# Optimization experiments

Hardware: AMD Instinct MI355X
Metric: run time of the kernel (lower is better)

Reference implementation:

```python
import jax, jax.numpy as jnp
import numpy as np

LN_EPS = 1e-5

def _layernorm(x, g, b):
    mu = jnp.mean(x, axis=-1, keepdims=True)
    var = jnp.mean(jnp.square(x - mu), axis=-1, keepdims=True)
    return (x - mu) * jax.lax.rsqrt(var + LN_EPS) * g + b

def setup_inputs() -> dict:
    key = jax.random.key(0)
    B, T, C = 8, 2048, 1024
    ks = jax.random.split(key, 16)
    s = 1.0 / np.sqrt(C)
    inp = {
        'x':   jax.random.normal(ks[0], (B, T, C), dtype=jnp.float32),
        'Wq':  jax.random.uniform(ks[1], (C, C), jnp.float32, -s, s),
        'bq':  jax.random.uniform(ks[2], (C,), jnp.float32, -s, s),
        'Wk':  jax.random.uniform(ks[3], (C, C), jnp.float32, -s, s),
        'bk':  jax.random.uniform(ks[4], (C,), jnp.float32, -s, s),
        'Wv':  jax.random.uniform(ks[5], (C, C), jnp.float32, -s, s),
        'bv':  jax.random.uniform(ks[6], (C,), jnp.float32, -s, s),
        'g1':  jnp.ones((C,), jnp.float32),
        'be1': jnp.zeros((C,), jnp.float32),
        'W1':  jax.random.uniform(ks[7], (C, C), jnp.float32, -s, s),
        'bf1': jax.random.uniform(ks[8], (C,), jnp.float32, -s, s),
        'W2':  jax.random.uniform(ks[9], (C, C), jnp.float32, -s, s),
        'bf2': jax.random.uniform(ks[10], (C,), jnp.float32, -s, s),
        'g2':  jnp.ones((C,), jnp.float32),
        'be2': jnp.zeros((C,), jnp.float32),
    }
    return inp

def reference(x, Wq, bq, Wk, bk, Wv, bv, g1, be1, W1, bf1, W2, bf2, g2, be2):
    B, T, C = x.shape
    q = x @ Wq + bq
    k = x @ Wk + bk
    v = x @ Wv + bv
    # FFT cross-correlation along time axis
    fq = jnp.fft.rfft(q, axis=1)
    fk = jnp.fft.rfft(k, axis=1)
    corr = jnp.fft.irfft(fq * jnp.conj(fk), n=T, axis=1)  # [B,T,C]
    weights = jax.nn.softmax(corr, axis=1)
    # einsum 'btd,btv->btd': weights * sum over v's channel dim
    attn = weights * jnp.sum(v, axis=-1, keepdims=True)
    x = _layernorm(x + attn, g1, be1)
    h = jax.nn.relu(x @ W1 + bf1) @ W2 + bf2
    x = _layernorm(x + h, g2, be2)
    return x
```

## Files before the change

### kernel.cpp

```cpp
#include <hip/hip_runtime.h>
#include <math.h>

#define B_DIM 8
#define T_DIM 2048
#define C_DIM 1024
#define BT_DIM (B_DIM * T_DIM)
#define FSZ ((size_t)BT_DIM * C_DIM)
#define LN_EPS 1e-5f

typedef __bf16 bf16x8 __attribute__((ext_vector_type(8)));
typedef _Float16 f16x8 __attribute__((ext_vector_type(8)));
typedef float f32x4 __attribute__((ext_vector_type(4)));

__device__ __forceinline__ unsigned short f2bf(float f) {
  __bf16 h = (__bf16)f;
  return __builtin_bit_cast(unsigned short, h);
}
__device__ __forceinline__ unsigned short f2h(float f) {
  _Float16 h = (_Float16)f;
  return __builtin_bit_cast(unsigned short, h);
}

__device__ __forceinline__ void gld16(const void* g, void* l) {
  __builtin_amdgcn_global_load_lds(
      (const __attribute__((address_space(1))) unsigned int*)g,
      (__attribute__((address_space(3))) unsigned int*)l, 16, 0, 0);
}

__device__ __forceinline__ int swz(int a) {
  return a ^ (((a >> 4) ^ (a >> 8)) & 15);
}

__device__ __forceinline__ int enc11(int f) {
  return ((f & 3) << 9) | (((f >> 2) & 3) << 7) | (((f >> 4) & 3) << 5) |
         (((f >> 6) & 3) << 3) | (((f >> 8) & 3) << 1) | ((f >> 10) & 1);
}

__global__ __launch_bounds__(256)
void cvt_split_f16_kernel(const float* __restrict__ x, unsigned short* __restrict__ hi,
                          unsigned short* __restrict__ lo) {
  size_t idx = ((size_t)blockIdx.x * 256 + threadIdx.x) * 4;
  float4 v = *(const float4*)(x + idx);
  float f[4] = {v.x, v.y, v.z, v.w};
  unsigned short hv[4], lv[4];
#pragma unroll
  for (int i = 0; i < 4; i++) {
    _Float16 hb = (_Float16)f[i];
    hv[i] = __builtin_bit_cast(unsigned short, hb);
    lv[i] = f2h(f[i] - (float)hb);
  }
  *(ushort4*)(hi + idx) = make_ushort4(hv[0], hv[1], hv[2], hv[3]);
  *(ushort4*)(lo + idx) = make_ushort4(lv[0], lv[1], lv[2], lv[3]);
}

__global__ __launch_bounds__(256)
void wtrans_f16_kernel(const float* __restrict__ W, unsigned short* __restrict__ Wt,
                       int K, int N) {
  __shared__ float tile[32][33];
  const int tid = threadIdx.x;
  const int tx = tid & 31, ty = tid >> 5;
  const int n0 = blockIdx.x * 32, k0 = blockIdx.y * 32;
#pragma unroll
  for (int i = 0; i < 4; i++) {
    int row = ty + i * 8;
    tile[row][tx] = W[(size_t)(k0 + row) * N + n0 + tx];
  }
  __syncthreads();
#pragma unroll
  for (int i = 0; i < 4; i++) {
    int row = ty + i * 8;
    Wt[(size_t)(n0 + row) * K + k0 + tx] = f2h(tile[tx][row]);
  }
}

__global__ __launch_bounds__(256)
void wtrans_kernel(const float* __restrict__ W, unsigned short* __restrict__ Wt,
                   int K, int N) {
  __shared__ float tile[32][33];
  const int tid = threadIdx.x;
  const int tx = tid & 31, ty = tid >> 5;
  const int n0 = blockIdx.x * 32, k0 = blockIdx.y * 32;
#pragma unroll
  for (int i = 0; i < 4; i++) {
    int row = ty + i * 8;
    tile[row][tx] = W[(size_t)(k0 + row) * N + n0 + tx];
  }
  __syncthreads();
#pragma unroll
  for (int i = 0; i < 4; i++) {
    int row = ty + i * 8;
    Wt[(size_t)(n0 + row) * K + k0 + tx] = f2bf(tile[tx][row]);
  }
}

__global__ __launch_bounds__(256)
void wv_rowsum_kernel(const float* __restrict__ Wv, const float* __restrict__ bv,
                      float* __restrict__ wvsum, float* __restrict__ bvsum) {
  const int r = blockIdx.x;
  const int tid = threadIdx.x;
  const float* src = (r < C_DIM) ? (Wv + (size_t)r * C_DIM) : bv;
  float4 t4 = *(const float4*)(src + (tid << 2));
  float s = t4.x + t4.y + t4.z + t4.w;
#pragma unroll
  for (int off = 32; off > 0; off >>= 1) s += __shfl_down(s, off);
  __shared__ float ps[4];
  if ((tid & 63) == 0) ps[tid >> 6] = s;
  __syncthreads();
  if (tid == 0) {
    float v = ps[0] + ps[1] + ps[2] + ps[3];
    if (r < C_DIM) wvsum[r] = v; else bvsum[0] = v;
  }
}

__global__ __launch_bounds__(256)
void sv_dot_kernel(const float* __restrict__ x, const float* __restrict__ wvsum,
                   const float* __restrict__ bvsum, float* __restrict__ sv) {
  const int r = blockIdx.x;
  const int tid = threadIdx.x;
  float4 a = *(const float4*)(x + (size_t)r * C_DIM + (tid << 2));
  float4 w = *(const float4*)(wvsum + (tid << 2));
  float s = a.x * w.x + a.y * w.y + a.z * w.z + a.w * w.w;
#pragma unroll
  for (int off = 32; off > 0; off >>= 1) s += __shfl_down(s, off);
  __shared__ float ps[4];
  if ((tid & 63) == 0) ps[tid >> 6] = s;
  __syncthreads();
  if (tid == 0) sv[r] = ps[0] + ps[1] + ps[2] + ps[3] + bvsum[0];
}

__global__ __launch_bounds__(256, 2)
void gemm_bf16_kernel(const __bf16* __restrict__ A, const __bf16* __restrict__ Bt,
                      const float* __restrict__ bias, float* Yf, unsigned short* Yb,
                      int K, int N, int do_relu) {
  __shared__ __align__(16) __bf16 As[128 * 32];
  __shared__ __align__(16) __bf16 Bs[128 * 32];
  const int tid = threadIdx.x;
  const int wave = tid >> 6, lane = tid & 63;
  const int wr = wave >> 1, wc = wave & 1;
  const int r15 = lane & 15, kq = lane >> 4;
  const int m0 = blockIdx.y * 128, n0 = blockIdx.x * 128;

  f32x4 acc[4][4] = {};

  for (int k0 = 0; k0 < K; k0 += 32) {
#pragma unroll
    for (int r = 0; r < 2; ++r) {
      int idx = r * 256 + tid;
      int row = idx >> 2;
      int ko = (idx & 3) ^ ((row >> 1) & 3);
      gld16(A + (size_t)(m0 + row) * K + k0 + ko * 8, &As[idx * 8]);
      gld16(Bt + (size_t)(n0 + row) * K + k0 + ko * 8, &Bs[idx * 8]);
    }
    __syncthreads();
    bf16x8 afr[4], bfr[4];
#pragma unroll
    for (int i = 0; i < 4; i++) {
      int ar = wr * 64 + i * 16 + r15;
      afr[i] = *(const bf16x8*)&As[(ar * 4 + (kq ^ ((ar >> 1) & 3))) * 8];
      int br = wc * 64 + i * 16 + r15;
      bfr[i] = *(const bf16x8*)&Bs[(br * 4 + (kq ^ ((br >> 1) & 3))) * 8];
    }
#pragma unroll
    for (int mi = 0; mi < 4; mi++)
#pragma unroll
      for (int ni = 0; ni < 4; ni++)
        acc[mi][ni] = __builtin_amdgcn_mfma_f32_16x16x32_bf16(afr[mi], bfr[ni], acc[mi][ni], 0, 0, 0);
    __syncthreads();
  }

  float bv[4];
#pragma unroll
  for (int ni = 0; ni < 4; ni++) bv[ni] = bias[n0 + wc * 64 + ni * 16 + r15];

#pragma unroll
  for (int mi = 0; mi < 4; mi++)
#pragma unroll
    for (int ni = 0; ni < 4; ni++) {
      const int n = n0 + wc * 64 + ni * 16 + r15;
#pragma unroll
      for (int r = 0; r < 4; r++) {
        const int m = m0 + wr * 64 + mi * 16 + kq * 4 + r;
        float v = acc[mi][ni][r] + bv[ni];
        if (do_relu) v = fmaxf(v, 0.f);
        if (Yf) Yf[(size_t)m * N + n] = v;
        if (Yb) Yb[(size_t)m * N + n] = f2bf(v);
      }
    }
}

__global__ __launch_bounds__(512, 2)
void gemm_qkT_f16_8ph_kernel(const _Float16* __restrict__ Ahi, const _Float16* __restrict__ Alo,
                             const _Float16* __restrict__ Bq, const _Float16* __restrict__ Bk,
                             const float* __restrict__ biasq, const float* __restrict__ biask,
                             float* __restrict__ Yq, float* __restrict__ Yk, int K, int N) {
  __shared__ __align__(16) _Float16 AhL[3][256 * 32];
  __shared__ __align__(16) _Float16 AlL[3][256 * 32];
  __shared__ __align__(16) _Float16 BqL[3][128 * 32];
  __shared__ __align__(16) _Float16 BkL[3][128 * 32];

  const int tid = threadIdx.x;
  const int wave = tid >> 6, lane = tid & 63;
  const int wr = wave >> 2, wc = wave & 3;
  const int r15 = lane & 15, kq = lane >> 4;
  const int m0 = blockIdx.y * 256, n0 = blockIdx.x * 128;
  const int NT = K >> 5;

  const int row_a0 = tid >> 2;
  const int row_a1 = row_a0 + 128;
  const int ch = tid & 3;
  const int ko0 = ch ^ ((row_a0 >> 1) & 3);
  const int ko1 = ch ^ ((row_a1 >> 1) & 3);
  const _Float16* agh0 = Ahi + (size_t)(m0 + row_a0) * K + ko0 * 8;
  const _Float16* agl0 = Alo + (size_t)(m0 + row_a0) * K + ko0 * 8;
  const _Float16* agh1 = Ahi + (size_t)(m0 + row_a1) * K + ko1 * 8;
  const _Float16* agl1 = Alo + (size_t)(m0 + row_a1) * K + ko1 * 8;
  const _Float16* bgq  = Bq  + (size_t)(n0 + row_a0) * K + ko0 * 8;
  const _Float16* bgk  = Bk  + (size_t)(n0 + row_a0) * K + ko0 * 8;

  const int ksel = kq ^ ((r15 >> 1) & 3);
  const int aoff = (wr * 128 + r15) * 32 + ksel * 8;
  const int boff = (wc * 32 + r15) * 32 + ksel * 8;

  f32x4 accq[8][2] = {};
  f32x4 acck[8][2] = {};

  gld16(agh0 + 0, &AhL[0][(size_t)tid * 8]);
  gld16(agl0 + 0, &AlL[0][(size_t)tid * 8]);
  gld16(agh1 + 0, &AhL[0][(size_t)(tid + 512) * 8]);
  gld16(agl1 + 0, &AlL[0][(size_t)(tid + 512) * 8]);
  gld16(bgq + 0, &BqL[0][(size_t)tid * 8]);
  gld16(bgk + 0, &BkL[0][(size_t)tid * 8]);
  gld16(agh0 + 32, &AhL[1][(size_t)tid * 8]);
  gld16(agl0 + 32, &AlL[1][(size_t)tid * 8]);
  gld16(agh1 + 32, &AhL[1][(size_t)(tid + 512) * 8]);
  gld16(agl1 + 32, &AlL[1][(size_t)(tid + 512) * 8]);
  gld16(bgq + 32, &BqL[1][(size_t)tid * 8]);
  gld16(bgk + 32, &BkL[1][(size_t)tid * 8]);

  int bR = 0;
  int bS = 2;

  for (int j = 0; j < NT; ++j) {
    if (j < NT - 1) {
      asm volatile("s_waitcnt vmcnt(6)" ::: "memory");
    } else {
      asm volatile("s_waitcnt vmcnt(0)" ::: "memory");
    }
    __builtin_amdgcn_s_barrier();
    __builtin_amdgcn_sched_barrier(0);

    const int kk = (j + 2) * 32;
    const bool doStage = (j + 2 < NT);

    f16x8 bqf[2], bkf[2];
#pragma unroll
    for (int ni = 0; ni < 2; ++ni) {
      bqf[ni] = *(const f16x8*)&BqL[bR][boff + ni * 512];
      bkf[ni] = *(const f16x8*)&BkL[bR][boff + ni * 512];
    }

#pragma unroll
    for (int p = 0; p < 4; ++p) {
      f16x8 ah0 = *(const f16x8*)&AhL[bR][aoff + (2 * p + 0) * 512];
      f16x8 al0 = *(const f16x8*)&AlL[bR][aoff + (2 * p + 0) * 512];
      f16x8 ah1 = *(const f16x8*)&AhL[bR][aoff + (2 * p + 1) * 512];
      f16x8 al1 = *(const f16x8*)&AlL[bR][aoff + (2 * p + 1) * 512];
      if (doStage) {
        if (p == 0) {
          gld16(agh0 + kk, &AhL[bS][(size_t)tid * 8]);
          gld16(agl0 + kk, &AlL[bS][(size_t)tid * 8]);
        }
        if (p == 1) {
          gld16(agh1 + kk, &AhL[bS][(size_t)(tid + 512) * 8]);
          gld16(agl1 + kk, &AlL[bS][(size_t)(tid + 512) * 8]);
        }
        if (p == 2) gld16(bgq + kk, &BqL[bS][(size_t)tid * 8]);
        if (p == 3) gld16(bgk + kk, &BkL[bS][(size_t)tid * 8]);
      }
      __builtin_amdgcn_s_barrier();
      asm volatile("s_waitcnt lgkmcnt(0)" ::: "memory");
      __builtin_amdgcn_sched_barrier(0);
      __builtin_amdgcn_s_setprio(1);
#pragma unroll
      for (int m2 = 0; m2 < 2; ++m2) {
        const int mi = 2 * p + m2;
        const f16x8 ahv = m2 ? ah1 : ah0;
        const f16x8 alv = m2 ? al1 : al0;
#pragma unroll
        for (int ni = 0; ni < 2; ++ni) {
          accq[mi][ni] = __builtin_amdgcn_mfma_f32_16x16x32_f16(ahv, bqf[ni], accq[mi][ni], 0, 0, 0);
          accq[mi][ni] = __builtin_amdgcn_mfma_f32_16x16x32_f16(alv, bqf[ni], accq[mi][ni], 0, 0, 0);
          acck[mi][ni] = __builtin_amdgcn_mfma_f32_16x16x32_f16(ahv, bkf[ni], acck[mi][ni], 0, 0, 0);
          acck[mi][ni] = __builtin_amdgcn_mfma_f32_16x16x32_f16(alv, bkf[ni], acck[mi][ni], 0, 0, 0);
        }
      }
      __builtin_amdgcn_s_setprio(0);
      __builtin_amdgcn_sched_barrier(0);
    }

    bR = (bR + 1 == 3) ? 0 : bR + 1;
    bS = (bS + 1 == 3) ? 0 : bS + 1;
  }

  float bvq[2], bvk[2];
#pragma unroll
  for (int ni = 0; ni < 2; ++ni) {
    bvq[ni] = biasq[n0 + wc * 32 + ni * 16 + r15];
    bvk[ni] = biask[n0 + wc * 32 + ni * 16 + r15];
  }

#pragma unroll
  for (int mi = 0; mi < 8; ++mi) {
    const int mbase = m0 + wr * 128 + mi * 16 + kq * 4;
    const int bb = mbase >> 11;
    const int t = mbase & (T_DIM - 1);
#pragma unroll
    for (int ni = 0; ni < 2; ++ni) {
      const int n = n0 + wc * 32 + ni * 16 + r15;
      const size_t o = ((size_t)bb * C_DIM + n) * T_DIM + t;
      *(float4*)(Yq + o) = make_float4(accq[mi][ni][0] + bvq[ni], accq[mi][ni][1] + bvq[ni],
                                       accq[mi][ni][2] + bvq[ni], accq[mi][ni][3] + bvq[ni]);
      *(float4*)(Yk + o) = make_float4(acck[mi][ni][0] + bvk[ni], acck[mi][ni][1] + bvk[ni],
                                       acck[mi][ni][2] + bvk[ni], acck[mi][ni][3] + bvk[ni]);
    }
  }
}

__device__ void fft_dif(float2* X, const float2* tw, int tid, float sgn) {
#pragma unroll
  for (int s = 0; s < 5; s++) {
    const int m = 512 >> (2 * s);
    const int jstep = 512 / m;
#pragma unroll
    for (int ii = 0; ii < 2; ii++) {
      const int i = tid + ii * 256;
      const int q = i & (m - 1);
      const int a0 = ((i - q) << 2) + q;
      float2 x0 = X[swz(a0)];
      float2 x1 = X[swz(a0 + m)];
      float2 x2 = X[swz(a0 + 2 * m)];
      float2 x3 = X[swz(a0 + 3 * m)];
      float2 t0 = make_float2(x0.x + x2.x, x0.y + x2.y);
      float2 t2 = make_float2(x0.x - x2.x, x0.y - x2.y);
      float2 t1 = make_float2(x1.x + x3.x, x1.y + x3.y);
      float2 t3 = make_float2(x1.x - x3.x, x1.y - x3.y);
      const float jx = -sgn * t3.y, jy = sgn * t3.x;
      float2 y0 = make_float2(t0.x + t1.x, t0.y + t1.y);
      float2 y1 = make_float2(t2.x + jx, t2.y + jy);
      float2 y2 = make_float2(t0.x - t1.x, t0.y - t1.y);
      float2 y3 = make_float2(t2.x - jx, t2.y - jy);
      const int j1 = q * jstep;
      float2 tv = tw[swz(j1)];
      const float c1 = tv.x, s1 = tv.y * sgn;
      const float c2 = c1 * c1 - s1 * s1, s2 = 2.f * c1 * s1;
      const float c3 = c2 * c1 - s2 * s1, s3 = c2 * s1 + s2 * c1;
      X[swz(a0)] = y0;
      X[swz(a0 + m)] = make_float2(c1 * y1.x - s1 * y1.y, c1 * y1.y + s1 * y1.x);
      X[swz(a0 + 2 * m)] = make_float2(c2 * y2.x - s2 * y2.y, c2 * y2.y + s2 * y2.x);
      X[swz(a0 + 3 * m)] = make_float2(c3 * y3.x - s3 * y3.y, c3 * y3.y + s3 * y3.x);
    }
    __syncthreads();
  }
#pragma unroll
  for (int ii = 0; ii < 4; ii++) {
    const int a = (tid + ii * 256) << 1;
    float2 u = X[swz(a)], v = X[swz(a + 1)];
    X[swz(a)] = make_float2(u.x + v.x, u.y + v.y);
    X[swz(a + 1)] = make_float2(u.x - v.x, u.y - v.y);
  }
  __syncthreads();
}

__device__ void fft_dit_inv(float2* X, const float2* tw, int tid) {
#pragma unroll
  for (int ii = 0; ii < 4; ii++) {
    const int a = (tid + ii * 256) << 1;
    float2 u = X[swz(a)], v = X[swz(a + 1)];
    X[swz(a)] = make_float2(u.x + v.x, u.y + v.y);
    X[swz(a + 1)] = make_float2(u.x - v.x, u.y - v.y);
  }
  __syncthreads();
#pragma unroll
  for (int s = 4; s >= 0; s--) {
    const int m = 512 >> (2 * s);
    const int jstep = 512 / m;
#pragma unroll
    for (int ii = 0; ii < 2; ii++) {
      const int i = tid + ii * 256;
      const int q = i & (m - 1);
      const int a0 = ((i - q) << 2) + q;
      float2 v0 = X[swz(a0)];
      float2 v1 = X[swz(a0 + m)];
      float2 v2 = X[swz(a0 + 2 * m)];
      float2 v3 = X[swz(a0 + 3 * m)];
      const int j1 = q * jstep;
      float2 tv = tw[swz(j1)];
      const float c1 = tv.x, s1 = tv.y;
      const float c2 = c1 * c1 - s1 * s1, s2 = 2.f * c1 * s1;
      const float c3 = c2 * c1 - s2 * s1, s3 = c2 * s1 + s2 * c1;
      float2 w1 = make_float2(c1 * v1.x - s1 * v1.y, c1 * v1.y + s1 * v1.x);
      float2 w2 = make_float2(c2 * v2.x - s2 * v2.y, c2 * v2.y + s2 * v2.x);
      float2 w3 = make_float2(c3 * v3.x - s3 * v3.y, c3 * v3.y + s3 * v3.x);
      float2 t0 = make_float2(v0.x + w2.x, v0.y + w2.y);
      float2 t2 = make_float2(v0.x - w2.x, v0.y - w2.y);
      float2 t1 = make_float2(w1.x + w3.x, w1.y + w3.y);
      float2 t3 = make_float2(w1.x - w3.x, w1.y - w3.y);
      const float jx = -t3.y, jy = t3.x;
      X[swz(a0)] = make_float2(t0.x + t1.x, t0.y + t1.y);
      X[swz(a0 + m)] = make_float2(t2.x + jx, t2.y + jy);
      X[swz(a0 + 2 * m)] = make_float2(t0.x - t1.x, t0.y - t1.y);
      X[swz(a0 + 3 * m)] = make_float2(t2.x - jx, t2.y - jy);
    }
    __syncthreads();
  }
}

__global__ __launch_bounds__(256)
void corr_fft_kernel(const float* qT, const float* kT, float* corrT,
                     float* __restrict__ Mv, float* __restrict__ Iv) {
  __shared__ float2 bA[2048];
  __shared__ float2 bB[2048];
  __shared__ float2 tw[512];
  __shared__ float2 red[4];
  const int tid = threadIdx.x;
  const int wave = tid >> 6, lane = tid & 63;
  const int b = blockIdx.y;
  const int c0 = blockIdx.x * 2;
  const float* q0 = qT + ((size_t)b * C_DIM + c0) * T_DIM;
  const float* k0p = kT + ((size_t)b * C_DIM + c0) * T_DIM;

#pragma unroll
  for (int jj = 0; jj < 2; jj++) {
    int j = tid + jj * 256;
    float sA, cA;
    __sincosf((float)j * (6.283185307179586f / 2048.0f), &sA, &cA);
    tw[swz(j)] = make_float2(cA, sA);
  }

#pragma unroll
  for (int jj = 0; jj < 8; jj++) {
    int t = tid + jj * 256;
    bA[swz(t)] = make_float2(q0[t], q0[t + T_DIM]);
    bB[swz(t)] = make_float2(k0p[t], k0p[t + T_DIM]);
  }
  __syncthreads();

  fft_dif(bA, tw, tid, -1.0f);
  fft_dif(bB, tw, tid, -1.0f);

#pragma unroll 1
  for (int f = tid; f <= 1024; f += 256) {
    const int g = (2048 - f) & 2047;
    const int p = swz(enc11(f));
    const int p2 = swz(enc11(g));
    float2 Zq = bA[p], Zq2 = bA[p2];
    float2 Zk = bB[p], Zk2 = bB[p2];
    float2 Aq = make_float2(0.5f * (Zq.x + Zq2.x), 0.5f * (Zq.y - Zq2.y));
    float2 Dq = make_float2(Zq.x - Zq2.x, Zq.y + Zq2.y);
    float2 Bq = make_float2(0.5f * Dq.y, -0.5f * Dq.x);
    float2 Ak = make_float2(0.5f * (Zk.x + Zk2.x), 0.5f * (Zk.y - Zk2.y));
    float2 Dk = make_float2(Zk.x - Zk2.x, Zk.y + Zk2.y);
    float2 Bk = make_float2(0.5f * Dk.y, -0.5f * Dk.x);
    float2 G = make_float2(Aq.x * Ak.x + Aq.y * Ak.y, Aq.y * Ak.x - Aq.x * Ak.y);
    float2 H = make_float2(Bq.x * Bk.x + Bq.y * Bk.y, Bq.y * Bk.x - Bq.x * Bk.y);
    bA[p] = make_float2(G.x - H.y, G.y + H.x);
    if (p2 != p) bA[p2] = make_float2(G.x + H.y, -G.y + H.x);
  }
  __syncthreads();

  fft_dit_inv(bA, tw, tid);

  float* o0 = corrT + ((size_t)b * C_DIM + c0) * T_DIM;
  const float sc = 1.0f / 2048.0f;
  float mx0 = -INFINITY, mx1 = -INFINITY;
#pragma unroll
  for (int jj = 0; jj < 8; jj++) {
    int t = tid + jj * 256;
    float2 o = bA[swz(t)];
    float v0 = o.x * sc, v1 = o.y * sc;
    o0[t] = v0;
    o0[t + T_DIM] = v1;
    mx0 = fmaxf(mx0, v0);
    mx1 = fmaxf(mx1, v1);
  }
#pragma unroll
  for (int off = 32; off > 0; off >>= 1) {
    mx0 = fmaxf(mx0, __shfl_down(mx0, off));
    mx1 = fmaxf(mx1, __shfl_down(mx1, off));
  }
  if (lane == 0) red[wave] = make_float2(mx0, mx1);
  __syncthreads();
  const float M0 = fmaxf(fmaxf(red[0].x, red[1].x), fmaxf(red[2].x, red[3].x));
  const float M1 = fmaxf(fmaxf(red[0].y, red[1].y), fmaxf(red[2].y, red[3].y));
  __syncthreads();
  float s0 = 0.f, s1 = 0.f;
#pragma unroll
  for (int jj = 0; jj < 8; jj++) {
    int t = tid + jj * 256;
    float2 o = bA[swz(t)];
    s0 += __expf(o.x * sc - M0);
    s1 += __expf(o.y * sc - M1);
  }
#pragma unroll
  for (int off = 32; off > 0; off >>= 1) {
    s0 += __shfl_down(s0, off);
    s1 += __shfl_down(s1, off);
  }
  if (lane == 0) red[wave] = make_float2(s0, s1);
  __syncthreads();
  if (tid == 0) {
    float S0 = red[0].x + red[1].x + red[2].x + red[3].x;
    float S1 = red[0].y + red[1].y + red[2].y + red[3].y;
    Mv[(size_t)b * C_DIM + c0] = M0;
    Mv[(size_t)b * C_DIM + c0 + 1] = M1;
    Iv[(size_t)b * C_DIM + c0] = 1.0f / S0;
    Iv[(size_t)b * C_DIM + c0 + 1] = 1.0f / S1;
  }
}

__global__ __launch_bounds__(256)
void attn_transpose_kernel(const float* __restrict__ corrT, const float* __restrict__ Mv,
                           const float* __restrict__ Iv, const float* __restrict__ sv,
                           float* __restrict__ attn) {
  __shared__ float tile[32][33];
  const int tid = threadIdx.x;
  const int tx = tid & 31, ty = tid >> 5;
  const int t0 = blockIdx.x * 32, c0 = blockIdx.y * 32, b = blockIdx.z;
  const float svv = sv[(size_t)b * T_DIM + t0 + tx];
#pragma unroll
  for (int i = 0; i < 4; i++) {
    const int c = c0 + ty + i * 8;
    const float M = Mv[(size_t)b * C_DIM + c];
    const float I = Iv[(size_t)b * C_DIM + c];
    float v = corrT[((size_t)b * C_DIM + c) * T_DIM + t0 + tx];
    tile[ty + i * 8][tx] = __expf(v - M) * I * svv;
  }
  __syncthreads();
#pragma unroll
  for (int i = 0; i < 4; i++) {
    const int t = t0 + ty + i * 8;
    attn[((size_t)b * T_DIM + t) * C_DIM + c0 + tx] = tile[tx][ty + i * 8];
  }
}

__global__ __launch_bounds__(256)
void add_ln_kernel(const float* __restrict__ A, const float* __restrict__ Bv,
                   const float* __restrict__ g, const float* __restrict__ be,
                   float* __restrict__ outf, unsigned short* outb) {
  const int r = blockIdx.x;
  const int tid = threadIdx.x;
  const size_t base = (size_t)r * C_DIM + (tid << 2);
  float4 a = *(const float4*)(A + base);
  float4 b = *(const float4*)(Bv + base);
  float x0 = a.x + b.x, x1 = a.y + b.y, x2 = a.z + b.z, x3 = a.w + b.w;
  float s = x0 + x1 + x2 + x3;
  float s2 = x0 * x0 + x1 * x1 + x2 * x2 + x3 * x3;
#pragma unroll
  for (int off = 32; off > 0; off >>= 1) {
    s += __shfl_down(s, off);
    s2 += __shfl_down(s2, off);
  }
  __shared__ float ps[4], ps2[4];
  if ((tid & 63) == 0) { ps[tid >> 6] = s; ps2[tid >> 6] = s2; }
  __syncthreads();
  float S = ps[0] + ps[1] + ps[2] + ps[3];
  float S2 = ps2[0] + ps2[1] + ps2[2] + ps2[3];
  const float mu = S * (1.0f / C_DIM);
  const float var = S2 * (1.0f / C_DIM) - mu * mu;
  const float rs = rsqrtf(var + LN_EPS);
  float4 gv = *(const float4*)(g + (tid << 2));
  float4 bev = *(const float4*)(be + (tid << 2));
  float o0 = (x0 - mu) * rs * gv.x + bev.x;
  float o1 = (x1 - mu) * rs * gv.y + bev.y;
  float o2 = (x2 - mu) * rs * gv.z + bev.z;
  float o3 = (x3 - mu) * rs * gv.w + bev.w;
  *(float4*)(outf + base) = make_float4(o0, o1, o2, o3);
  if (outb) *(ushort4*)(outb + base) = make_ushort4(f2bf(o0), f2bf(o1), f2bf(o2), f2bf(o3));
}

extern "C" void kernel_launch(void* const* d_in, const int* in_sizes, int n_in,
                              void* d_out, int out_size, void* d_ws, size_t ws_size,
                              hipStream_t stream) {
  const float* x   = (const float*)d_in[0];
  const float* Wq  = (const float*)d_in[1];
  const float* bq  = (const float*)d_in[2];
  const float* Wk  = (const float*)d_in[3];
  const float* bk  = (const float*)d_in[4];
  const float* Wv  = (const float*)d_in[5];
  const float* bv  = (const float*)d_in[6];
  const float* g1  = (const float*)d_in[7];
  const float* be1 = (const float*)d_in[8];
  const float* W1  = (const float*)d_in[9];
  const float* bf1 = (const float*)d_in[10];
  const float* W2  = (const float*)d_in[11];
  const float* bf2 = (const float*)d_in[12];
  const float* g2  = (const float*)d_in[13];
  const float* be2 = (const float*)d_in[14];
  float* out = (float*)d_out;

  float* ws = (float*)d_ws;
  float* qbuf = ws;
  float* kbuf = ws + FSZ;
  unsigned short* xhi = (unsigned short*)(ws + 2 * FSZ);
  unsigned short* xlo = xhi + FSZ;
  unsigned short* wA = xlo + FSZ;
  unsigned short* wB = wA + (size_t)C_DIM * C_DIM;
  float* sv = (float*)(wB + (size_t)C_DIM * C_DIM);
  float* wvsum = sv + BT_DIM;
  float* bvsum = wvsum + C_DIM;
  float* Mv = bvsum + 1;
  float* Iv = Mv + (size_t)B_DIM * C_DIM;

  const dim3 blk(256);
  const dim3 ggrid(C_DIM / 128, BT_DIM / 128);
  const dim3 qkgrid(C_DIM / 128, BT_DIM / 256);
  const dim3 tgrid(C_DIM / 32, C_DIM / 32);

  cvt_split_f16_kernel<<<dim3(FSZ / 1024), blk, 0, stream>>>(x, xhi, xlo);

  wv_rowsum_kernel<<<dim3(C_DIM + 1), blk, 0, stream>>>(Wv, bv, wvsum, bvsum);
  sv_dot_kernel<<<dim3(BT_DIM), blk, 0, stream>>>(x, wvsum, bvsum, sv);

  wtrans_f16_kernel<<<tgrid, blk, 0, stream>>>(Wq, wA, C_DIM, C_DIM);
  wtrans_f16_kernel<<<tgrid, blk, 0, stream>>>(Wk, wB, C_DIM, C_DIM);
  gemm_qkT_f16_8ph_kernel<<<qkgrid, dim3(512), 0, stream>>>(
      (const _Float16*)xhi, (const _Float16*)xlo,
      (const _Float16*)wA, (const _Float16*)wB,
      bq, bk, qbuf, kbuf, C_DIM, C_DIM);

  corr_fft_kernel<<<dim3(C_DIM / 2, B_DIM), blk, 0, stream>>>(qbuf, kbuf, qbuf, Mv, Iv);

  attn_transpose_kernel<<<dim3(T_DIM / 32, C_DIM / 32, B_DIM), blk, 0, stream>>>(
      qbuf, Mv, Iv, sv, kbuf);

  add_ln_kernel<<<dim3(BT_DIM), blk, 0, stream>>>(x, kbuf, g1, be1, qbuf, xhi);

  wtrans_kernel<<<tgrid, blk, 0, stream>>>(W1, wA, C_DIM, C_DIM);
  wtrans_kernel<<<tgrid, blk, 0, stream>>>(W2, wB, C_DIM, C_DIM);

  gemm_bf16_kernel<<<ggrid, blk, 0, stream>>>((const __bf16*)xhi, (const __bf16*)wA,
                                              bf1, nullptr, xlo, C_DIM, C_DIM, 1);
  gemm_bf16_kernel<<<ggrid, blk, 0, stream>>>((const __bf16*)xlo, (const __bf16*)wB,
                                              bf2, kbuf, nullptr, C_DIM, C_DIM, 0);

  add_ln_kernel<<<dim3(BT_DIM), blk, 0, stream>>>(qbuf, kbuf, g2, be2, out, nullptr);
}
```

Baseline: 581.7 us.

## Fuse sv dot into split conversion, attn into LN1, and remap GEMM tiles for XCD locality

The sv dot product now runs inside the fp16 hi/lo split kernel, so x is read once there instead of twice. The softmax-normalise/transpose pass is merged with the first residual add and LayerNorm, staging a 32x1024 tile in shared memory so the attn intermediate never goes to global memory. Both GEMM kernels remap block indices so each XCD works on a compact M/N region for better L2 reuse. The fused attn_ln kernel uses about 128KB of LDS per block, which limits occupancy, and its corrT reads are column-strided. Buffer roles for the second GEMM and the final LayerNorm are swapped to match.

```diff
diff --git a/kernel.cpp b/kernel.cpp
--- a/kernel.cpp
+++ b/kernel.cpp
@@ -37,10 +37,15 @@
 }
 
 __global__ __launch_bounds__(256)
-void cvt_split_f16_kernel(const float* __restrict__ x, unsigned short* __restrict__ hi,
-                          unsigned short* __restrict__ lo) {
-  size_t idx = ((size_t)blockIdx.x * 256 + threadIdx.x) * 4;
-  float4 v = *(const float4*)(x + idx);
+void cvt_split_sv_kernel(const float* __restrict__ x, const float* __restrict__ wvsum,
+                         const float* __restrict__ bvsum,
+                         unsigned short* __restrict__ hi, unsigned short* __restrict__ lo,
+                         float* __restrict__ sv) {
+  const int r = blockIdx.x;
+  const int tid = threadIdx.x;
+  const size_t base = (size_t)r * C_DIM + (tid << 2);
+  float4 v = *(const float4*)(x + base);
+  float4 w = *(const float4*)(wvsum + (tid << 2));
   float f[4] = {v.x, v.y, v.z, v.w};
   unsigned short hv[4], lv[4];
 #pragma unroll
@@ -49,8 +54,15 @@
     hv[i] = __builtin_bit_cast(unsigned short, hb);
     lv[i] = f2h(f[i] - (float)hb);
   }
-  *(ushort4*)(hi + idx) = make_ushort4(hv[0], hv[1], hv[2], hv[3]);
-  *(ushort4*)(lo + idx) = make_ushort4(lv[0], lv[1], lv[2], lv[3]);
+  *(ushort4*)(hi + base) = make_ushort4(hv[0], hv[1], hv[2], hv[3]);
+  *(ushort4*)(lo + base) = make_ushort4(lv[0], lv[1], lv[2], lv[3]);
+  float s = v.x * w.x + v.y * w.y + v.z * w.z + v.w * w.w;
+#pragma unroll
+  for (int off = 32; off > 0; off >>= 1) s += __shfl_down(s, off);
+  __shared__ float ps[4];
+  if ((tid & 63) == 0) ps[tid >> 6] = s;
+  __syncthreads();
+  if (tid == 0) sv[r] = ps[0] + ps[1] + ps[2] + ps[3] + bvsum[0];
 }
 
 __global__ __launch_bounds__(256)
@@ -110,22 +122,6 @@
     float v = ps[0] + ps[1] + ps[2] + ps[3];
     if (r < C_DIM) wvsum[r] = v; else bvsum[0] = v;
   }
-}
-
-__global__ __launch_bounds__(256)
-void sv_dot_kernel(const float* __restrict__ x, const float* __restrict__ wvsum,
-                   const float* __restrict__ bvsum, float* __restrict__ sv) {
-  const int r = blockIdx.x;
-  const int tid = threadIdx.x;
-  float4 a = *(const float4*)(x + (size_t)r * C_DIM + (tid << 2));
-  float4 w = *(const float4*)(wvsum + (tid << 2));
-  float s = a.x * w.x + a.y * w.y + a.z * w.z + a.w * w.w;
-#pragma unroll
-  for (int off = 32; off > 0; off >>= 1) s += __shfl_down(s, off);
-  __shared__ float ps[4];
-  if ((tid & 63) == 0) ps[tid >> 6] = s;
-  __syncthreads();
-  if (tid == 0) sv[r] = ps[0] + ps[1] + ps[2] + ps[3] + bvsum[0];
 }
 
 __global__ __launch_bounds__(256, 2)
@@ -138,7 +134,11 @@
   const int wave = tid >> 6, lane = tid & 63;
   const int wr = wave >> 1, wc = wave & 1;
   const int r15 = lane & 15, kq = lane >> 4;
-  const int m0 = blockIdx.y * 128, n0 = blockIdx.x * 128;
+  const int h = blockIdx.y * 8 + blockIdx.x;
+  const int xcd = h & 7, s = h >> 3;
+  const int mIdx = (xcd << 4) + (s & 7) + ((s >> 6) << 3);
+  const int nIdx = (s >> 3) & 7;
+  const int m0 = mIdx * 128, n0 = nIdx * 128;
 
   f32x4 acc[4][4] = {};
 
@@ -202,7 +202,11 @@
   const int wave = tid >> 6, lane = tid & 63;
   const int wr = wave >> 2, wc = wave & 3;
   const int r15 = lane & 15, kq = lane >> 4;
-  const int m0 = blockIdx.y * 256, n0 = blockIdx.x * 128;
+  const int h = blockIdx.y * 8 + blockIdx.x;
+  const int xcd = h & 7, s = h >> 3;
+  const int mIdx = (xcd << 3) + (s & 3) + ((s >> 5) << 2);
+  const int nIdx = (s >> 2) & 7;
+  const int m0 = mIdx * 256, n0 = nIdx * 128;
   const int NT = K >> 5;
 
   const int row_a0 = tid >> 2;
@@ -518,28 +522,70 @@
   }
 }
 
-__global__ __launch_bounds__(256)
-void attn_transpose_kernel(const float* __restrict__ corrT, const float* __restrict__ Mv,
-                           const float* __restrict__ Iv, const float* __restrict__ sv,
-                           float* __restrict__ attn) {
-  __shared__ float tile[32][33];
-  const int tid = threadIdx.x;
-  const int tx = tid & 31, ty = tid >> 5;
-  const int t0 = blockIdx.x * 32, c0 = blockIdx.y * 32, b = blockIdx.z;
-  const float svv = sv[(size_t)b * T_DIM + t0 + tx];
-#pragma unroll
-  for (int i = 0; i < 4; i++) {
-    const int c = c0 + ty + i * 8;
-    const float M = Mv[(size_t)b * C_DIM + c];
-    const float I = Iv[(size_t)b * C_DIM + c];
-    float v = corrT[((size_t)b * C_DIM + c) * T_DIM + t0 + tx];
-    tile[ty + i * 8][tx] = __expf(v - M) * I * svv;
-  }
-  __syncthreads();
-#pragma unroll
-  for (int i = 0; i < 4; i++) {
-    const int t = t0 + ty + i * 8;
-    attn[((size_t)b * T_DIM + t) * C_DIM + c0 + tx] = tile[tx][ty + i * 8];
+__global__ __launch_bounds__(512)
+void attn_ln_kernel(const float* __restrict__ corrT, const float* __restrict__ Mv,
+                    const float* __restrict__ Iv, const float* __restrict__ sv,
+                    const float* __restrict__ x, const float* __restrict__ g,
+                    const float* __restrict__ be, float* __restrict__ outf,
+                    unsigned short* __restrict__ outb) {
+  __shared__ float att[32][1028];
+  const int tid = threadIdx.x;
+  const int b = blockIdx.y;
+  const int t0 = blockIdx.x * 32;
+
+  const int tx = tid & 31;
+  const int cy = tid >> 5;
+  const float* cb = corrT + (size_t)b * C_DIM * T_DIM + t0 + tx;
+  const float* Mb = Mv + (size_t)b * C_DIM;
+  const float* Ib = Iv + (size_t)b * C_DIM;
+#pragma unroll 8
+  for (int it = 0; it < 64; ++it) {
+    const int c = cy + (it << 4);
+    float v = cb[(size_t)c * T_DIM];
+    att[tx][c] = __expf(v - Mb[c]) * Ib[c];
+  }
+  __syncthreads();
+
+  const int t = tid >> 4;
+  const int l16 = tid & 15;
+  const float svv = sv[(size_t)b * T_DIM + t0 + t];
+  const float* xr = x + ((size_t)b * T_DIM + t0 + t) * C_DIM;
+  float s = 0.f, s2 = 0.f;
+#pragma unroll
+  for (int j = 0; j < 16; ++j) {
+    const int c = (l16 + (j << 4)) << 2;
+    float4 xv = *(const float4*)(xr + c);
+    float4 av = *(const float4*)&att[t][c];
+    float v0 = xv.x + av.x * svv;
+    float v1 = xv.y + av.y * svv;
+    float v2 = xv.z + av.z * svv;
+    float v3 = xv.w + av.w * svv;
+    *(float4*)&att[t][c] = make_float4(v0, v1, v2, v3);
+    s += v0 + v1 + v2 + v3;
+    s2 += v0 * v0 + v1 * v1 + v2 * v2 + v3 * v3;
+  }
+#pragma unroll
+  for (int off = 8; off > 0; off >>= 1) {
+    s += __shfl_xor(s, off);
+    s2 += __shfl_xor(s2, off);
+  }
+  const float mu = s * (1.0f / C_DIM);
+  const float var = s2 * (1.0f / C_DIM) - mu * mu;
+  const float rs = rsqrtf(var + LN_EPS);
+  float* orow = outf + ((size_t)b * T_DIM + t0 + t) * C_DIM;
+  unsigned short* obrow = outb + ((size_t)b * T_DIM + t0 + t) * C_DIM;
+#pragma unroll
+  for (int j = 0; j < 16; ++j) {
+    const int c = (l16 + (j << 4)) << 2;
+    float4 val = *(const float4*)&att[t][c];
+    float4 gv = *(const float4*)(g + c);
+    float4 bev = *(const float4*)(be + c);
+    float o0 = (val.x - mu) * rs * gv.x + bev.x;
+    float o1 = (val.y - mu) * rs * gv.y + bev.y;
+    float o2 = (val.z - mu) * rs * gv.z + bev.z;
+    float o3 = (val.w - mu) * rs * gv.w + bev.w;
+    *(float4*)(orow + c) = make_float4(o0, o1, o2, o3);
+    *(ushort4*)(obrow + c) = make_ushort4(f2bf(o0), f2bf(o1), f2bf(o2), f2bf(o3));
   }
 }
 
@@ -616,10 +662,9 @@
   const dim3 qkgrid(C_DIM / 128, BT_DIM / 256);
   const dim3 tgrid(C_DIM / 32, C_DIM / 32);
 
-  cvt_split_f16_kernel<<<dim3(FSZ / 1024), blk, 0, stream>>>(x, xhi, xlo);
-
   wv_rowsum_kernel<<<dim3(C_DIM + 1), blk, 0, stream>>>(Wv, bv, wvsum, bvsum);
-  sv_dot_kernel<<<dim3(BT_DIM), blk, 0, stream>>>(x, wvsum, bvsum, sv);
+
+  cvt_split_sv_kernel<<<dim3(BT_DIM), blk, 0, stream>>>(x, wvsum, bvsum, xhi, xlo, sv);
 
   wtrans_f16_kernel<<<tgrid, blk, 0, stream>>>(Wq, wA, C_DIM, C_DIM);
   wtrans_f16_kernel<<<tgrid, blk, 0, stream>>>(Wk, wB, C_DIM, C_DIM);
@@ -630,10 +675,8 @@
 
   corr_fft_kernel<<<dim3(C_DIM / 2, B_DIM), blk, 0, stream>>>(qbuf, kbuf, qbuf, Mv, Iv);
 
-  attn_transpose_kernel<<<dim3(T_DIM / 32, C_DIM / 32, B_DIM), blk, 0, stream>>>(
-      qbuf, Mv, Iv, sv, kbuf);
-
-  add_ln_kernel<<<dim3(BT_DIM), blk, 0, stream>>>(x, kbuf, g1, be1, qbuf, xhi);
+  attn_ln_kernel<<<dim3(T_DIM / 32, B_DIM), dim3(512), 0, stream>>>(
+      qbuf, Mv, Iv, sv, x, g1, be1, kbuf, xhi);
 
   wtrans_kernel<<<tgrid, blk, 0, stream>>>(W1, wA, C_DIM, C_DIM);
   wtrans_kernel<<<tgrid, blk, 0, stream>>>(W2, wB, C_DIM, C_DIM);
@@ -641,7 +684,7 @@
   gemm_bf16_kernel<<<ggrid, blk, 0, stream>>>((const __bf16*)xhi, (const __bf16*)wA,
                                               bf1, nullptr, xlo, C_DIM, C_DIM, 1);
   gemm_bf16_kernel<<<ggrid, blk, 0, stream>>>((const __bf16*)xlo, (const __bf16*)wB,
-                                              bf2, kbuf, nullptr, C_DIM, C_DIM, 0);
-
-  add_ln_kernel<<<dim3(BT_DIM), blk, 0, stream>>>(qbuf, kbuf, g2, be2, out, nullptr);
-}
+                                              bf2, qbuf, nullptr, C_DIM, C_DIM, 0);
+
+  add_ln_kernel<<<dim3(BT_DIM), blk, 0, stream>>>(kbuf, qbuf, g2, be2, out, nullptr);
+}
```

Measured after the change: 522.5 us. 1.11x faster.
